# Kernel optimization log

Hardware: AMD Instinct MI355X
Metric: run time of the kernel (lower is better)

## Reference

```python
import jax, jax.numpy as jnp
import numpy as np

K = 5          # receptive field
N_IN = 4       # inputs per LUT node
DEPTH = 2      # tree depth -> layer widths [16, 4, 1]


def lut_nodes(s, lut):
    """Differentiable DWN LUT nodes.
    s:   [P, C, N, n] selected inputs in [0,1]
    lut: [C, N, 2**n] raw LUT weights (sigmoid applied -> entries in (0,1))
    out[p,c,m] = sum_a sigmoid(lut[c,m,a]) * prod_j s_j^{bit_j(a)} (1-s_j)^{1-bit_j(a)}
    Evaluated by contracting one address bit at a time (bit j=0 most significant).
    """
    n = s.shape[-1]
    C, N = lut.shape[0], lut.shape[1]
    t = jax.nn.sigmoid(lut).reshape((C, N) + (2,) * n)  # [C,N,2,...,2]
    for j in reversed(range(n)):
        xb = s[..., j].reshape(s.shape[:-1] + (1,) * j)  # [P,C,N,1*j]
        t = t[..., 0] * (1.0 - xb) + t[..., 1] * xb
    return t  # [P, C, N]


def extract_patches(x):
    """nn.Unfold(kernel=K, stride=1, pad=0): x [B,Cin,H,W] -> [B*P, Cin*K*K]."""
    B, Cin, H, W = x.shape
    Hp, Wp = H - K + 1, W - K + 1
    cols = jnp.stack([x[:, :, i:i + Hp, j:j + Wp]
                      for i in range(K) for j in range(K)], axis=2)  # [B,Cin,K*K,Hp,Wp]
    patches = cols.reshape(B, Cin * K * K, Hp * Wp)
    return patches.transpose(0, 2, 1).reshape(B * Hp * Wp, Cin * K * K), (B, Hp, Wp)


def setup_inputs() -> dict:
    key = jax.random.key(0)
    ks = jax.random.split(key, 7)
    C = 64
    return {
        "x": jax.random.uniform(ks[0], (32, 1, 32, 32), dtype=jnp.float32),
        "lut0": jax.random.normal(ks[1], (C, 16, 16), dtype=jnp.float32),
        "lut1": jax.random.normal(ks[2], (C, 4, 16), dtype=jnp.float32),
        "lut2": jax.random.normal(ks[3], (C, 1, 16), dtype=jnp.float32),
        "idx0": jax.random.randint(ks[4], (C, 16, N_IN), 0, 25, dtype=jnp.int32),
        "idx1": jax.random.randint(ks[5], (C, 4, N_IN), 0, 16, dtype=jnp.int32),
        "idx2": jax.random.randint(ks[6], (C, 1, N_IN), 0, 4, dtype=jnp.int32),
    }


def reference(x, lut0, lut1, lut2, idx0, idx1, idx2):
    patches, (B, Hp, Wp) = extract_patches(x)          # [P, 25]
    C = lut0.shape[0]
    # layer 0: gather raw patch features per channel/node
    s0 = patches[:, idx0]                              # [P, C, 16, 4]
    h0 = lut_nodes(s0, lut0)                           # [P, C, 16]
    # layer 1: per-channel gather from previous layer
    s1 = jnp.take_along_axis(h0[:, :, None, :], idx1[None], axis=-1)  # [P, C, 4, 4]
    h1 = lut_nodes(s1, lut1)                           # [P, C, 4]
    # layer 2 (root)
    s2 = jnp.take_along_axis(h1[:, :, None, :], idx2[None], axis=-1)  # [P, C, 1, 4]
    h2 = lut_nodes(s2, lut2)[..., 0]                   # [P, C]
    out = h2.reshape(B, Hp * Wp, C).transpose(0, 2, 1).reshape(B, C, Hp, Wp)
    return out
```

## Files before the change

kernel.cpp:

```cpp
#include <hip/hip_runtime.h>
#include <math.h>

#define KK 5
#define WPOUT 28
#define PPI 784
#define NCH 64
#define NPAIR 12544
#define THREADS 256
#define NNODE 21

typedef float f32x32 __attribute__((ext_vector_type(32)));
typedef float f32x16 __attribute__((ext_vector_type(16)));
typedef _Float16 h2  __attribute__((ext_vector_type(2)));
typedef unsigned u32x8 __attribute__((ext_vector_type(8)));

static __device__ __forceinline__ h2 u2h(unsigned u) { return __builtin_bit_cast(h2, u); }
static __device__ __forceinline__ unsigned h2u(h2 h) { return __builtin_bit_cast(unsigned, h); }
static __device__ __forceinline__ unsigned f2u(float f) { return __builtin_bit_cast(unsigned, f); }
static __device__ __forceinline__ float u2f(unsigned u) { return __builtin_bit_cast(float, u); }

static __device__ __forceinline__ unsigned packpair(float a, float b) {
    const auto pk = __builtin_amdgcn_cvt_pkrtz(a, b);
    return __builtin_bit_cast(unsigned, pk);
}

static __device__ __forceinline__ unsigned pkfma_ed(unsigned s, unsigned X) {
    unsigned r;
    asm("v_pk_fma_f16 %0, %1, %2, %2 op_sel:[0,1,0] op_sel_hi:[1,1,0]"
        : "=v"(r) : "v"(s), "s"(X));
    return r;
}

static __device__ __forceinline__ unsigned node_pair_s(const u32x8 ED,
                                                       unsigned s0, unsigned s1,
                                                       unsigned s2, unsigned s3) {
    unsigned v[8];
#pragma unroll
    for (int k = 0; k < 8; ++k) v[k] = pkfma_ed(s3, ED[k]);
    const h2 s2h = u2h(s2), s1h = u2h(s1), s0h = u2h(s0);
    h2 w[4];
#pragma unroll
    for (int k = 0; k < 4; ++k) {
        const h2 ve = u2h(v[2 * k]), vo = u2h(v[2 * k + 1]);
        w[k] = s2h * (vo - ve) + ve;
    }
    const h2 u0 = s1h * (w[1] - w[0]) + w[0];
    const h2 u1 = s1h * (w[3] - w[2]) + w[2];
    return h2u(s0h * (u1 - u0) + u0);
}

__global__ void sigmoid_prep(const float* __restrict__ lut0,
                             const float* __restrict__ lut1,
                             const float* __restrict__ lut2,
                             unsigned* __restrict__ ws)
{
    const int t = blockIdx.x * 256 + threadIdx.x;
    if (t >= NCH * NNODE * 8) return;
    const int k    = t & 7;
    const int node = (t >> 3) % NNODE;
    const int c    = t / (8 * NNODE);
    const float* src;
    if (node < 16)      src = lut0 + (c * 16 + node) * 16;
    else if (node < 20) src = lut1 + (c * 4 + (node - 16)) * 16;
    else                src = lut2 + c * 16;
    const float a = src[2 * k], b = src[2 * k + 1];
    const float ea = 1.0f / (1.0f + __expf(-a));
    const float eb = 1.0f / (1.0f + __expf(-b));
    const _Float16 e = (_Float16)ea;
    const _Float16 d = (_Float16)(eb - ea);
    ws[(c * NNODE + node) * 8 + k] =
        (unsigned)__builtin_bit_cast(unsigned short, e) |
        ((unsigned)__builtin_bit_cast(unsigned short, d) << 16);
}

__global__ __launch_bounds__(THREADS)
void dwn_conv_lut_kernel(const float* __restrict__ x,
                         const unsigned* __restrict__ ws,
                         const int*   __restrict__ idx0,
                         const int*   __restrict__ idx1,
                         const int*   __restrict__ idx2,
                         float*       __restrict__ out)
{
    const int tid = threadIdx.x;
    const int c   = blockIdx.y;

    const int pi = blockIdx.x * THREADS + tid;
    const int p  = 2 * pi;
    const int b  = p / PPI;
    const int q  = p - b * PPI;
    const int i  = q / WPOUT;
    const int j  = q - i * WPOUT;

    const float* rp0 = x + b * 1024 + i * 32 + j;
    f32x32 pv;
#pragma unroll
    for (int di = 0; di < KK; ++di) {
        const float2* r2 = (const float2*)(rp0 + di * 32);
        const float2 w01 = r2[0], w23 = r2[1], w45 = r2[2];
        const float w[6] = { w01.x, w01.y, w23.x, w23.y, w45.x, w45.y };
#pragma unroll
        for (int dj = 0; dj < KK; ++dj) {
            pv[di * 5 + dj] = u2f(packpair(w[dj], w[dj + 1]));
        }
    }

    const unsigned* lutc = ws + c * (NNODE * 8);
    const int* id0 = idx0 + c * 64;

    f32x16 h0;
#pragma unroll
    for (int m = 0; m < 16; ++m) {
        const u32x8 ED = *(const u32x8*)(lutc + m * 8);
        const int i0 = __builtin_amdgcn_readfirstlane(id0[m * 4 + 0]);
        const int i1 = __builtin_amdgcn_readfirstlane(id0[m * 4 + 1]);
        const int i2 = __builtin_amdgcn_readfirstlane(id0[m * 4 + 2]);
        const int i3 = __builtin_amdgcn_readfirstlane(id0[m * 4 + 3]);
        h0[m] = u2f(node_pair_s(ED, f2u(pv[i0]), f2u(pv[i1]), f2u(pv[i2]), f2u(pv[i3])));
    }

    const int* id1 = idx1 + c * 16;
    unsigned h1[4];
#pragma unroll
    for (int m = 0; m < 4; ++m) {
        const u32x8 ED = *(const u32x8*)(lutc + (16 + m) * 8);
        const int i0 = __builtin_amdgcn_readfirstlane(id1[m * 4 + 0]);
        const int i1 = __builtin_amdgcn_readfirstlane(id1[m * 4 + 1]);
        const int i2 = __builtin_amdgcn_readfirstlane(id1[m * 4 + 2]);
        const int i3 = __builtin_amdgcn_readfirstlane(id1[m * 4 + 3]);
        h1[m] = node_pair_s(ED, f2u(h0[i0]), f2u(h0[i1]), f2u(h0[i2]), f2u(h0[i3]));
    }

    const int* id2 = idx2 + c * 4;
    unsigned s[4];
#pragma unroll
    for (int jj = 0; jj < 4; ++jj) {
        const int ii = __builtin_amdgcn_readfirstlane(id2[jj]);
        s[jj] = (ii == 0) ? h1[0] : (ii == 1) ? h1[1] : (ii == 2) ? h1[2] : h1[3];
    }
    const u32x8 ED2 = *(const u32x8*)(lutc + 20 * 8);
    const h2 r = u2h(node_pair_s(ED2, s[0], s[1], s[2], s[3]));

    float2* o = (float2*)(out + (b * NCH + c) * PPI + q);
    *o = make_float2((float)r[0], (float)r[1]);
}

extern "C" void kernel_launch(void* const* d_in, const int* in_sizes, int n_in,
                              void* d_out, int out_size, void* d_ws, size_t ws_size,
                              hipStream_t stream) {
    const float* x    = (const float*)d_in[0];
    const float* lut0 = (const float*)d_in[1];
    const float* lut1 = (const float*)d_in[2];
    const float* lut2 = (const float*)d_in[3];
    const int*   idx0 = (const int*)d_in[4];
    const int*   idx1 = (const int*)d_in[5];
    const int*   idx2 = (const int*)d_in[6];
    float* out = (float*)d_out;
    unsigned* ws = (unsigned*)d_ws;

    {
        const int total = NCH * NNODE * 8;
        sigmoid_prep<<<dim3((total + 255) / 256), dim3(256), 0, stream>>>(lut0, lut1, lut2, ws);
    }
    {
        dim3 grid(NPAIR / THREADS, NCH);
        dwn_conv_lut_kernel<<<grid, dim3(THREADS), 0, stream>>>(x, ws, idx0, idx1, idx2, out);
    }
}
```

Before: 27.46 us.

## Fuse sigmoid LUT prep into main kernel and broadcast tables via readlane

Removes the separate sigmoid_prep launch. Each wavefront now computes the packed fp16 sigmoid LUT entries itself, one per lane across three registers, and loads the index tables into lanes. Values are then broadcast to scalars with v_readlane instead of scalar memory loads through a workspace. This drops one kernel launch and the global round trip, at the cost of redundant sigmoid computation in every wave and many readlane instructions. It also adds a launch-bounds occupancy hint.

Result: slower. 28.56 us (+4.0%).

```diff
diff --git a/kernel.cpp b/kernel.cpp
--- a/kernel.cpp
+++ b/kernel.cpp
@@ -12,7 +12,6 @@
 typedef float f32x32 __attribute__((ext_vector_type(32)));
 typedef float f32x16 __attribute__((ext_vector_type(16)));
 typedef _Float16 h2  __attribute__((ext_vector_type(2)));
-typedef unsigned u32x8 __attribute__((ext_vector_type(8)));
 
 static __device__ __forceinline__ h2 u2h(unsigned u) { return __builtin_bit_cast(h2, u); }
 static __device__ __forceinline__ unsigned h2u(h2 h) { return __builtin_bit_cast(unsigned, h); }
@@ -31,9 +30,9 @@
     return r;
 }
 
-static __device__ __forceinline__ unsigned node_pair_s(const u32x8 ED,
-                                                       unsigned s0, unsigned s1,
-                                                       unsigned s2, unsigned s3) {
+static __device__ __forceinline__ unsigned node_ed(const unsigned ED[8],
+                                                   unsigned s0, unsigned s1,
+                                                   unsigned s2, unsigned s3) {
     unsigned v[8];
 #pragma unroll
     for (int k = 0; k < 8; ++k) v[k] = pkfma_ed(s3, ED[k]);
@@ -49,16 +48,11 @@
     return h2u(s0h * (u1 - u0) + u0);
 }
 
-__global__ void sigmoid_prep(const float* __restrict__ lut0,
-                             const float* __restrict__ lut1,
-                             const float* __restrict__ lut2,
-                             unsigned* __restrict__ ws)
-{
-    const int t = blockIdx.x * 256 + threadIdx.x;
-    if (t >= NCH * NNODE * 8) return;
-    const int k    = t & 7;
-    const int node = (t >> 3) % NNODE;
-    const int c    = t / (8 * NNODE);
+static __device__ __forceinline__ unsigned ed_for(int t, int c,
+                                                  const float* __restrict__ lut0,
+                                                  const float* __restrict__ lut1,
+                                                  const float* __restrict__ lut2) {
+    const int node = t >> 3, k = t & 7;
     const float* src;
     if (node < 16)      src = lut0 + (c * 16 + node) * 16;
     else if (node < 20) src = lut1 + (c * 4 + (node - 16)) * 16;
@@ -68,21 +62,32 @@
     const float eb = 1.0f / (1.0f + __expf(-b));
     const _Float16 e = (_Float16)ea;
     const _Float16 d = (_Float16)(eb - ea);
-    ws[(c * NNODE + node) * 8 + k] =
-        (unsigned)__builtin_bit_cast(unsigned short, e) |
-        ((unsigned)__builtin_bit_cast(unsigned short, d) << 16);
+    return (unsigned)__builtin_bit_cast(unsigned short, e) |
+           ((unsigned)__builtin_bit_cast(unsigned short, d) << 16);
 }
 
-__global__ __launch_bounds__(THREADS)
+#define RL(v, l) ((unsigned)__builtin_amdgcn_readlane((int)(v), (l)))
+
+__global__ __launch_bounds__(THREADS, 4)
 void dwn_conv_lut_kernel(const float* __restrict__ x,
-                         const unsigned* __restrict__ ws,
+                         const float* __restrict__ lut0,
+                         const float* __restrict__ lut1,
+                         const float* __restrict__ lut2,
                          const int*   __restrict__ idx0,
                          const int*   __restrict__ idx1,
                          const int*   __restrict__ idx2,
                          float*       __restrict__ out)
 {
-    const int tid = threadIdx.x;
-    const int c   = blockIdx.y;
+    const int tid  = threadIdx.x;
+    const int c    = blockIdx.y;
+    const int lane = tid & 63;
+
+    const unsigned ed0 = ed_for(lane,       c, lut0, lut1, lut2);
+    const unsigned ed1 = ed_for(lane + 64,  c, lut0, lut1, lut2);
+    const unsigned ed2 = ed_for(lane + 128, c, lut0, lut1, lut2);
+    const int ix0 = idx0[c * 64 + lane];
+    const int ix1 = (lane < 16) ? idx1[c * 16 + lane]
+                  : (lane < 20) ? idx2[c * 4 + (lane - 16)] : 0;
 
     const int pi = blockIdx.x * THREADS + tid;
     const int p  = 2 * pi;
@@ -104,41 +109,43 @@
         }
     }
 
-    const unsigned* lutc = ws + c * (NNODE * 8);
-    const int* id0 = idx0 + c * 64;
-
     f32x16 h0;
 #pragma unroll
     for (int m = 0; m < 16; ++m) {
-        const u32x8 ED = *(const u32x8*)(lutc + m * 8);
-        const int i0 = __builtin_amdgcn_readfirstlane(id0[m * 4 + 0]);
-        const int i1 = __builtin_amdgcn_readfirstlane(id0[m * 4 + 1]);
-        const int i2 = __builtin_amdgcn_readfirstlane(id0[m * 4 + 2]);
-        const int i3 = __builtin_amdgcn_readfirstlane(id0[m * 4 + 3]);
-        h0[m] = u2f(node_pair_s(ED, f2u(pv[i0]), f2u(pv[i1]), f2u(pv[i2]), f2u(pv[i3])));
+        unsigned ED[8];
+#pragma unroll
+        for (int k = 0; k < 8; ++k)
+            ED[k] = (m < 8) ? RL(ed0, m * 8 + k) : RL(ed1, (m - 8) * 8 + k);
+        const int i0 = (int)RL(ix0, 4 * m + 0);
+        const int i1 = (int)RL(ix0, 4 * m + 1);
+        const int i2 = (int)RL(ix0, 4 * m + 2);
+        const int i3 = (int)RL(ix0, 4 * m + 3);
+        h0[m] = u2f(node_ed(ED, f2u(pv[i0]), f2u(pv[i1]), f2u(pv[i2]), f2u(pv[i3])));
     }
 
-    const int* id1 = idx1 + c * 16;
     unsigned h1[4];
 #pragma unroll
     for (int m = 0; m < 4; ++m) {
-        const u32x8 ED = *(const u32x8*)(lutc + (16 + m) * 8);
-        const int i0 = __builtin_amdgcn_readfirstlane(id1[m * 4 + 0]);
-        const int i1 = __builtin_amdgcn_readfirstlane(id1[m * 4 + 1]);
-        const int i2 = __builtin_amdgcn_readfirstlane(id1[m * 4 + 2]);
-        const int i3 = __builtin_amdgcn_readfirstlane(id1[m * 4 + 3]);
-        h1[m] = node_pair_s(ED, f2u(h0[i0]), f2u(h0[i1]), f2u(h0[i2]), f2u(h0[i3]));
+        unsigned ED[8];
+#pragma unroll
+        for (int k = 0; k < 8; ++k) ED[k] = RL(ed2, m * 8 + k);
+        const int i0 = (int)RL(ix1, 4 * m + 0);
+        const int i1 = (int)RL(ix1, 4 * m + 1);
+        const int i2 = (int)RL(ix1, 4 * m + 2);
+        const int i3 = (int)RL(ix1, 4 * m + 3);
+        h1[m] = node_ed(ED, f2u(h0[i0]), f2u(h0[i1]), f2u(h0[i2]), f2u(h0[i3]));
     }
 
-    const int* id2 = idx2 + c * 4;
     unsigned s[4];
 #pragma unroll
     for (int jj = 0; jj < 4; ++jj) {
-        const int ii = __builtin_amdgcn_readfirstlane(id2[jj]);
+        const int ii = (int)RL(ix1, 16 + jj);
         s[jj] = (ii == 0) ? h1[0] : (ii == 1) ? h1[1] : (ii == 2) ? h1[2] : h1[3];
     }
-    const u32x8 ED2 = *(const u32x8*)(lutc + 20 * 8);
-    const h2 r = u2h(node_pair_s(ED2, s[0], s[1], s[2], s[3]));
+    unsigned ED2[8];
+#pragma unroll
+    for (int k = 0; k < 8; ++k) ED2[k] = RL(ed2, 32 + k);
+    const h2 r = u2h(node_ed(ED2, s[0], s[1], s[2], s[3]));
 
     float2* o = (float2*)(out + (b * NCH + c) * PPI + q);
     *o = make_float2((float)r[0], (float)r[1]);
@@ -155,14 +162,9 @@
     const int*   idx1 = (const int*)d_in[5];
     const int*   idx2 = (const int*)d_in[6];
     float* out = (float*)d_out;
-    unsigned* ws = (unsigned*)d_ws;
 
-    {
-        const int total = NCH * NNODE * 8;
-        sigmoid_prep<<<dim3((total + 255) / 256), dim3(256), 0, stream>>>(lut0, lut1, lut2, ws);
-    }
-    {
-        dim3 grid(NPAIR / THREADS, NCH);
-        dwn_conv_lut_kernel<<<grid, dim3(THREADS), 0, stream>>>(x, ws, idx0, idx1, idx2, out);
-    }
+    dim3 grid(NPAIR / THREADS, NCH);
+    dim3 block(THREADS);
+    dwn_conv_lut_kernel<<<grid, block, 0, stream>>>(x, lut0, lut1, lut2,
+                                                    idx0, idx1, idx2, out);
 }
```
